# Kernel tuning notes

Measured on AMD Instinct MI355X. Metric: run time of the kernel, lower is better.

The kernel has to match this reference:

```python
import jax, jax.numpy as jnp
import numpy as np

# Constants from GaussianSplattingCompliance.__init__
SCALE_MIN, SCALE_MAX = 0.05, 1.5
RATIO_MIN, RATIO_MAX = 0.5, 3.5
ROT_MIN, ROT_MAX = -np.pi / 2, np.pi / 2
AXIS_OFFSET = 0.05
EMIN = 1e-9
SMOOTH_K = 10.0

N_POINTS = 131072  # number of FE element centers (512x256 mesh, flattened)
N_G = 256          # number of gaussians (args['args']['N_g'])


def setup_inputs() -> dict:
    key = jax.random.key(0)
    k0, k1, k2, k3, k4 = jax.random.split(key, 5)
    coords = jax.random.uniform(k0, (N_POINTS, 2), dtype=jnp.float32)
    W_scale = jax.random.normal(k1, (N_G, 1), dtype=jnp.float32)
    W_shape_var = jax.random.normal(k2, (N_G, 1), dtype=jnp.float32)
    W_rotation = jax.random.normal(k3, (N_G, 1), dtype=jnp.float32)
    W_offsets = jax.random.normal(k4, (N_G, 2), dtype=jnp.float32)
    return {"coords": coords, "W_scale": W_scale, "W_shape_var": W_shape_var,
            "W_rotation": W_rotation, "W_offsets": W_offsets}


def reference(coords, W_scale, W_shape_var, W_rotation, W_offsets):
    # coord bounds are constant buffers in the original module (computed once in __init__)
    c = jax.lax.stop_gradient(coords)
    cmin, cmax = c.min(axis=0), c.max(axis=0)                      # (2,)
    coord_min = cmin - cmax * AXIS_OFFSET
    coord_max = cmax + cmax * AXIS_OFFSET

    B = W_scale.shape[0]
    base_scale = (SCALE_MAX - SCALE_MIN) * jax.nn.sigmoid(W_scale)[:, 0] + SCALE_MIN   # (B,)
    ratio = (RATIO_MAX - RATIO_MIN) * jax.nn.sigmoid(W_shape_var) + RATIO_MIN          # (B,1)
    sigmas = jnp.concatenate([jnp.ones((B, 1), coords.dtype), ratio], axis=1)          # (B,2)
    rotation = ROT_MIN + (ROT_MAX - ROT_MIN) * jax.nn.sigmoid(W_rotation)[:, 0]        # (B,)
    offsets = coord_min + (coord_max - coord_min) * jax.nn.sigmoid(W_offsets)          # (B,2)

    cos_r, sin_r = jnp.cos(rotation), jnp.sin(rotation)
    R = jnp.stack([jnp.stack([cos_r, -sin_r], axis=-1),
                   jnp.stack([sin_r, cos_r], axis=-1)], axis=-2)                       # (B,2,2)
    inv_cov_diag = 1.0 / (sigmas ** 2 + 1e-6)                                          # (B,2)

    # (B, N, 2): centered, scaled coordinates per gaussian
    xy = (coords[None, :, :] - offsets[:, None, :]) / (base_scale[:, None, None] + 1e-8)
    rxy = jnp.einsum('bij,bnj->bni', R, xy)                                            # (B,N,2)
    # diagonal Mahalanobis quadratic form
    z = jnp.sqrt(jnp.einsum('bni,bi,bni->bn', rxy, inv_cov_diag, rxy))                 # (B,N)
    kernel = jax.nn.sigmoid(-10.0 * (z - 1.0))                                         # 1/(1+exp(10(z-1)))
    kernel_sum = kernel.sum(axis=0) + 1e-8                                             # (N,)
    H = (1.0 - EMIN) * jax.nn.sigmoid(-SMOOTH_K * (kernel_sum - 0.5)) + EMIN           # (N,)
    return H
```

## Files before the change

### kernel.cpp

```cpp
#include <hip/hip_runtime.h>
#include <cmath>

#define N_GAUSS 256

__global__ __launch_bounds__(256) void k_partial_minmax(
    const float2* __restrict__ coords, int n, float4* __restrict__ partial) {
  int tid = blockIdx.x * blockDim.x + threadIdx.x;
  int stride = gridDim.x * blockDim.x;
  float mnx = INFINITY, mny = INFINITY, mxx = -INFINITY, mxy = -INFINITY;
  for (int i = tid; i < n; i += stride) {
    float2 c = coords[i];
    mnx = fminf(mnx, c.x);
    mny = fminf(mny, c.y);
    mxx = fmaxf(mxx, c.x);
    mxy = fmaxf(mxy, c.y);
  }
  for (int o = 32; o > 0; o >>= 1) {
    mnx = fminf(mnx, __shfl_down(mnx, o));
    mny = fminf(mny, __shfl_down(mny, o));
    mxx = fmaxf(mxx, __shfl_down(mxx, o));
    mxy = fmaxf(mxy, __shfl_down(mxy, o));
  }
  __shared__ float4 lds[4];
  if ((threadIdx.x & 63) == 0) lds[threadIdx.x >> 6] = make_float4(mnx, mny, mxx, mxy);
  __syncthreads();
  if (threadIdx.x == 0) {
    float4 r = lds[0];
    for (int w = 1; w < 4; ++w) {
      float4 o = lds[w];
      r.x = fminf(r.x, o.x);
      r.y = fminf(r.y, o.y);
      r.z = fmaxf(r.z, o.z);
      r.w = fmaxf(r.w, o.w);
    }
    partial[blockIdx.x] = r;
  }
}

__device__ __forceinline__ float sigmoidf_fast(float w) {
  float t = __builtin_amdgcn_exp2f(-1.4426950408889634f * w);
  return 1.0f / (1.0f + t);
}

__global__ __launch_bounds__(256) void k_fused_main(
    const float2* __restrict__ coords,
    const float4* __restrict__ partial,
    const float* __restrict__ W_scale,
    const float* __restrict__ W_shape_var,
    const float* __restrict__ W_rotation,
    const float* __restrict__ W_offsets,
    float* __restrict__ out, int n) {
  __shared__ float4 sp[2 * N_GAUSS];
  __shared__ float4 lds4[4];
  __shared__ float4 boundsS;

  int t = threadIdx.x;

  float4 r = partial[t];
  for (int o = 32; o > 0; o >>= 1) {
    r.x = fminf(r.x, __shfl_down(r.x, o));
    r.y = fminf(r.y, __shfl_down(r.y, o));
    r.z = fmaxf(r.z, __shfl_down(r.z, o));
    r.w = fmaxf(r.w, __shfl_down(r.w, o));
  }
  if ((t & 63) == 0) lds4[t >> 6] = r;
  __syncthreads();
  if (t == 0) {
    float4 a = lds4[0];
    for (int w = 1; w < 4; ++w) {
      float4 o = lds4[w];
      a.x = fminf(a.x, o.x);
      a.y = fminf(a.y, o.y);
      a.z = fmaxf(a.z, o.z);
      a.w = fmaxf(a.w, o.w);
    }
    boundsS = a;
  }
  __syncthreads();
  float4 bc = boundsS;

  {
    float cmin0 = bc.x - bc.z * 0.05f;
    float cmin1 = bc.y - bc.w * 0.05f;
    float cmax0 = bc.z + bc.z * 0.05f;
    float cmax1 = bc.w + bc.w * 0.05f;

    float sS = sigmoidf_fast(W_scale[t]);
    float base_scale = 1.45f * sS + 0.05f;
    float sV = sigmoidf_fast(W_shape_var[t]);
    float ratio = 3.0f * sV + 0.5f;
    float sR = sigmoidf_fast(W_rotation[t]);
    const float PIf = 3.14159265358979323846f;
    float rot = -0.5f * PIf + PIf * sR;
    float sOx = sigmoidf_fast(W_offsets[2 * t]);
    float sOy = sigmoidf_fast(W_offsets[2 * t + 1]);
    float ox = cmin0 + (cmax0 - cmin0) * sOx;
    float oy = cmin1 + (cmax1 - cmin1) * sOy;

    float cr = cosf(rot), sr = sinf(rot);
    float inv_s = 1.0f / (base_scale + 1e-8f);
    float r0 = rsqrtf(1.0f + 1e-6f);
    float r1 = rsqrtf(fmaf(ratio, ratio, 1e-6f));

    float A = r0 * cr * inv_s;
    float B = -r0 * sr * inv_s;
    float E = -fmaf(A, ox, B * oy);
    float C = r1 * sr * inv_s;
    float D = r1 * cr * inv_s;
    float F = -fmaf(C, ox, D * oy);

    sp[2 * t]     = make_float4(A, B, E, C);
    sp[2 * t + 1] = make_float4(D, F, 0.0f, 0.0f);
  }
  __syncthreads();

  int i = blockIdx.x * blockDim.x + threadIdx.x;
  if (i >= n) return;
  float2 c = coords[i];
  float x = c.x, y = c.y;
  float ks = 1e-8f;
  const float K1 = 14.4269504088896339f;

  for (int b0 = 0; b0 < N_GAUSS; b0 += 8) {
#pragma unroll
    for (int j = 0; j < 8; ++j) {
      int b = b0 + j;
      float4 p0 = sp[2 * b];
      float4 p1 = sp[2 * b + 1];
      float u = fmaf(p0.x, x, fmaf(p0.y, y, p0.z));
      float v = fmaf(p0.w, x, fmaf(p1.x, y, p1.y));
      float z = sqrtf(fmaf(u, u, v * v));
      float tt = __builtin_amdgcn_exp2f(fmaf(K1, z, -K1));
      ks += __builtin_amdgcn_rcpf(1.0f + tt);
    }
    if (__all(ks > 6.0f)) break;
  }

  float t2 = __builtin_amdgcn_exp2f(fmaf(K1, ks, -0.5f * K1));
  float s = __builtin_amdgcn_rcpf(1.0f + t2);
  out[i] = fmaf(1e-9f, 1.0f - s, s);
}

extern "C" void kernel_launch(void* const* d_in, const int* in_sizes, int n_in,
                              void* d_out, int out_size, void* d_ws, size_t ws_size,
                              hipStream_t stream) {
  const float* coords      = (const float*)d_in[0];
  const float* W_scale     = (const float*)d_in[1];
  const float* W_shape_var = (const float*)d_in[2];
  const float* W_rotation  = (const float*)d_in[3];
  const float* W_offsets   = (const float*)d_in[4];
  float* out = (float*)d_out;

  int n = in_sizes[0] / 2;

  float4* partial = (float4*)d_ws;

  k_partial_minmax<<<256, 256, 0, stream>>>((const float2*)coords, n, partial);
  int blocks = (n + 255) / 256;
  k_fused_main<<<blocks, 256, 0, stream>>>((const float2*)coords, partial,
                                           W_scale, W_shape_var, W_rotation,
                                           W_offsets, out, n);
}
```

Measured before the change: 66.84 us.

## Fuse min/max reduction and main pass into one cooperative kernel with grid sync

Replaces the two-kernel sequence (partial min/max, then fused evaluation) with a single cooperative launch of at most 512 blocks. Each block writes its partial bounds, a grid-wide sync follows, and then every block reduces all partials, folds the gaussian parameters into LDS and grid-strides over the points. This removes one kernel launch and the gap between launches. In exchange it pays for a grid barrier, has each block redo the final reduction and parameter setup, and caps parallelism at 512 blocks, so each thread handles several points.

Result: slower. 126.8 us (+89.7%).

```diff
diff --git a/kernel.cpp b/kernel.cpp
--- a/kernel.cpp
+++ b/kernel.cpp
@@ -1,45 +1,203 @@
 #include <hip/hip_runtime.h>
+#include <hip/hip_cooperative_groups.h>
 #include <cmath>
 
 #define N_GAUSS 256
+
+namespace cg = cooperative_groups;
+
+
+__device__ __forceinline__ float sigmoidf_fast(float w) {
+  float t = __builtin_amdgcn_exp2f(-1.4426950408889634f * w);
+  return 1.0f / (1.0f + t);
+}
+
+__device__ __forceinline__ void wave_reduce_minmax(float4& r) {
+  for (int o = 32; o > 0; o >>= 1) {
+    r.x = fminf(r.x, __shfl_down(r.x, o));
+    r.y = fminf(r.y, __shfl_down(r.y, o));
+    r.z = fmaxf(r.z, __shfl_down(r.z, o));
+    r.w = fmaxf(r.w, __shfl_down(r.w, o));
+  }
+}
+
+__device__ __forceinline__ void store_agent(float* p, float v) {
+  __hip_atomic_store(p, v, __ATOMIC_RELAXED, __HIP_MEMORY_SCOPE_AGENT);
+}
+__device__ __forceinline__ float load_agent(const float* p) {
+  return __hip_atomic_load(p, __ATOMIC_RELAXED, __HIP_MEMORY_SCOPE_AGENT);
+}
+
+__device__ __forceinline__ void fold_params(float4 bc, int t,
+    const float* __restrict__ W_scale, const float* __restrict__ W_shape_var,
+    const float* __restrict__ W_rotation, const float* __restrict__ W_offsets,
+    float4* sp) {
+  float cmin0 = bc.x - bc.z * 0.05f;
+  float cmin1 = bc.y - bc.w * 0.05f;
+  float cmax0 = bc.z + bc.z * 0.05f;
+  float cmax1 = bc.w + bc.w * 0.05f;
+
+  float sS = sigmoidf_fast(W_scale[t]);
+  float base_scale = 1.45f * sS + 0.05f;
+  float sV = sigmoidf_fast(W_shape_var[t]);
+  float ratio = 3.0f * sV + 0.5f;
+  float sR = sigmoidf_fast(W_rotation[t]);
+  const float PIf = 3.14159265358979323846f;
+  float rot = -0.5f * PIf + PIf * sR;
+  float sOx = sigmoidf_fast(W_offsets[2 * t]);
+  float sOy = sigmoidf_fast(W_offsets[2 * t + 1]);
+  float ox = cmin0 + (cmax0 - cmin0) * sOx;
+  float oy = cmin1 + (cmax1 - cmin1) * sOy;
+
+  float cr = cosf(rot), sr = sinf(rot);
+  float inv_s = 1.0f / (base_scale + 1e-8f);
+  float r0 = rsqrtf(1.0f + 1e-6f);
+  float r1 = rsqrtf(fmaf(ratio, ratio, 1e-6f));
+
+  float A = r0 * cr * inv_s;
+  float B = -r0 * sr * inv_s;
+  float E = -fmaf(A, ox, B * oy);
+  float C = r1 * sr * inv_s;
+  float D = r1 * cr * inv_s;
+  float F = -fmaf(C, ox, D * oy);
+
+  sp[2 * t]     = make_float4(A, B, E, C);
+  sp[2 * t + 1] = make_float4(D, F, 0.0f, 0.0f);
+}
+
+__device__ __forceinline__ float eval_point(const float4* sp, float2 c) {
+  float x = c.x, y = c.y;
+  float ks = 1e-8f;
+  const float K1 = 14.4269504088896339f;
+
+  for (int b0 = 0; b0 < N_GAUSS; b0 += 8) {
+#pragma unroll
+    for (int j = 0; j < 8; ++j) {
+      int b = b0 + j;
+      float4 p0 = sp[2 * b];
+      float4 p1 = sp[2 * b + 1];
+      float u = fmaf(p0.x, x, fmaf(p0.y, y, p0.z));
+      float v = fmaf(p0.w, x, fmaf(p1.x, y, p1.y));
+      float z = sqrtf(fmaf(u, u, v * v));
+      float tt = __builtin_amdgcn_exp2f(fmaf(K1, z, -K1));
+      ks += __builtin_amdgcn_rcpf(1.0f + tt);
+    }
+    if (__all(ks > 6.0f)) break;
+  }
+
+  float t2 = __builtin_amdgcn_exp2f(fmaf(K1, ks, -0.5f * K1));
+  float s = __builtin_amdgcn_rcpf(1.0f + t2);
+  return fmaf(1e-9f, 1.0f - s, s);
+}
+
+__global__ __launch_bounds__(256) void k_coop(
+    const float2* __restrict__ coords,
+    float* __restrict__ pbuf,
+    const float* __restrict__ W_scale,
+    const float* __restrict__ W_shape_var,
+    const float* __restrict__ W_rotation,
+    const float* __restrict__ W_offsets,
+    float* __restrict__ out, int n) {
+  __shared__ float4 sp[2 * N_GAUSS];
+  __shared__ float4 lds4[4];
+  __shared__ float4 boundsS;
+
+  int t = threadIdx.x;
+  int nb = gridDim.x;
+  int nthreads = nb * 256;
+  int gid = blockIdx.x * 256 + t;
+
+  float4 r = make_float4(INFINITY, INFINITY, -INFINITY, -INFINITY);
+  for (int i = gid; i < n; i += nthreads) {
+    float2 c = coords[i];
+    r.x = fminf(r.x, c.x);
+    r.y = fminf(r.y, c.y);
+    r.z = fmaxf(r.z, c.x);
+    r.w = fmaxf(r.w, c.y);
+  }
+  wave_reduce_minmax(r);
+  if ((t & 63) == 0) lds4[t >> 6] = r;
+  __syncthreads();
+  if (t == 0) {
+    float4 a = lds4[0];
+    for (int w = 1; w < 4; ++w) {
+      float4 o = lds4[w];
+      a.x = fminf(a.x, o.x);
+      a.y = fminf(a.y, o.y);
+      a.z = fmaxf(a.z, o.z);
+      a.w = fmaxf(a.w, o.w);
+    }
+    store_agent(&pbuf[4 * blockIdx.x + 0], a.x);
+    store_agent(&pbuf[4 * blockIdx.x + 1], a.y);
+    store_agent(&pbuf[4 * blockIdx.x + 2], a.z);
+    store_agent(&pbuf[4 * blockIdx.x + 3], a.w);
+  }
+
+  cg::this_grid().sync();
+
+  float4 g = make_float4(INFINITY, INFINITY, -INFINITY, -INFINITY);
+  for (int s = t; s < nb; s += 256) {
+    float px = load_agent(&pbuf[4 * s + 0]);
+    float py = load_agent(&pbuf[4 * s + 1]);
+    float pz = load_agent(&pbuf[4 * s + 2]);
+    float pw = load_agent(&pbuf[4 * s + 3]);
+    g.x = fminf(g.x, px);
+    g.y = fminf(g.y, py);
+    g.z = fmaxf(g.z, pz);
+    g.w = fmaxf(g.w, pw);
+  }
+  wave_reduce_minmax(g);
+  if ((t & 63) == 0) lds4[t >> 6] = g;
+  __syncthreads();
+  if (t == 0) {
+    float4 a = lds4[0];
+    for (int w = 1; w < 4; ++w) {
+      float4 o = lds4[w];
+      a.x = fminf(a.x, o.x);
+      a.y = fminf(a.y, o.y);
+      a.z = fmaxf(a.z, o.z);
+      a.w = fmaxf(a.w, o.w);
+    }
+    boundsS = a;
+  }
+  __syncthreads();
+  float4 bc = boundsS;
+
+  fold_params(bc, t, W_scale, W_shape_var, W_rotation, W_offsets, sp);
+  __syncthreads();
+
+  for (int i = gid; i < n; i += nthreads) {
+    out[i] = eval_point(sp, coords[i]);
+  }
+}
 
 __global__ __launch_bounds__(256) void k_partial_minmax(
     const float2* __restrict__ coords, int n, float4* __restrict__ partial) {
   int tid = blockIdx.x * blockDim.x + threadIdx.x;
   int stride = gridDim.x * blockDim.x;
-  float mnx = INFINITY, mny = INFINITY, mxx = -INFINITY, mxy = -INFINITY;
+  float4 r = make_float4(INFINITY, INFINITY, -INFINITY, -INFINITY);
   for (int i = tid; i < n; i += stride) {
     float2 c = coords[i];
-    mnx = fminf(mnx, c.x);
-    mny = fminf(mny, c.y);
-    mxx = fmaxf(mxx, c.x);
-    mxy = fmaxf(mxy, c.y);
-  }
-  for (int o = 32; o > 0; o >>= 1) {
-    mnx = fminf(mnx, __shfl_down(mnx, o));
-    mny = fminf(mny, __shfl_down(mny, o));
-    mxx = fmaxf(mxx, __shfl_down(mxx, o));
-    mxy = fmaxf(mxy, __shfl_down(mxy, o));
-  }
+    r.x = fminf(r.x, c.x);
+    r.y = fminf(r.y, c.y);
+    r.z = fmaxf(r.z, c.x);
+    r.w = fmaxf(r.w, c.y);
+  }
+  wave_reduce_minmax(r);
   __shared__ float4 lds[4];
-  if ((threadIdx.x & 63) == 0) lds[threadIdx.x >> 6] = make_float4(mnx, mny, mxx, mxy);
+  if ((threadIdx.x & 63) == 0) lds[threadIdx.x >> 6] = r;
   __syncthreads();
   if (threadIdx.x == 0) {
-    float4 r = lds[0];
+    float4 a = lds[0];
     for (int w = 1; w < 4; ++w) {
       float4 o = lds[w];
-      r.x = fminf(r.x, o.x);
-      r.y = fminf(r.y, o.y);
-      r.z = fmaxf(r.z, o.z);
-      r.w = fmaxf(r.w, o.w);
-    }
-    partial[blockIdx.x] = r;
-  }
-}
-
-__device__ __forceinline__ float sigmoidf_fast(float w) {
-  float t = __builtin_amdgcn_exp2f(-1.4426950408889634f * w);
-  return 1.0f / (1.0f + t);
+      a.x = fminf(a.x, o.x);
+      a.y = fminf(a.y, o.y);
+      a.z = fmaxf(a.z, o.z);
+      a.w = fmaxf(a.w, o.w);
+    }
+    partial[blockIdx.x] = a;
+  }
 }
 
 __global__ __launch_bounds__(256) void k_fused_main(
@@ -57,12 +215,7 @@
   int t = threadIdx.x;
 
   float4 r = partial[t];
-  for (int o = 32; o > 0; o >>= 1) {
-    r.x = fminf(r.x, __shfl_down(r.x, o));
-    r.y = fminf(r.y, __shfl_down(r.y, o));
-    r.z = fmaxf(r.z, __shfl_down(r.z, o));
-    r.w = fmaxf(r.w, __shfl_down(r.w, o));
-  }
+  wave_reduce_minmax(r);
   if ((t & 63) == 0) lds4[t >> 6] = r;
   __syncthreads();
   if (t == 0) {
@@ -79,72 +232,18 @@
   __syncthreads();
   float4 bc = boundsS;
 
-  {
-    float cmin0 = bc.x - bc.z * 0.05f;
-    float cmin1 = bc.y - bc.w * 0.05f;
-    float cmax0 = bc.z + bc.z * 0.05f;
-    float cmax1 = bc.w + bc.w * 0.05f;
-
-    float sS = sigmoidf_fast(W_scale[t]);
-    float base_scale = 1.45f * sS + 0.05f;
-    float sV = sigmoidf_fast(W_shape_var[t]);
-    float ratio = 3.0f * sV + 0.5f;
-    float sR = sigmoidf_fast(W_rotation[t]);
-    const float PIf = 3.14159265358979323846f;
-    float rot = -0.5f * PIf + PIf * sR;
-    float sOx = sigmoidf_fast(W_offsets[2 * t]);
-    float sOy = sigmoidf_fast(W_offsets[2 * t + 1]);
-    float ox = cmin0 + (cmax0 - cmin0) * sOx;
-    float oy = cmin1 + (cmax1 - cmin1) * sOy;
-
-    float cr = cosf(rot), sr = sinf(rot);
-    float inv_s = 1.0f / (base_scale + 1e-8f);
-    float r0 = rsqrtf(1.0f + 1e-6f);
-    float r1 = rsqrtf(fmaf(ratio, ratio, 1e-6f));
-
-    float A = r0 * cr * inv_s;
-    float B = -r0 * sr * inv_s;
-    float E = -fmaf(A, ox, B * oy);
-    float C = r1 * sr * inv_s;
-    float D = r1 * cr * inv_s;
-    float F = -fmaf(C, ox, D * oy);
-
-    sp[2 * t]     = make_float4(A, B, E, C);
-    sp[2 * t + 1] = make_float4(D, F, 0.0f, 0.0f);
-  }
+  fold_params(bc, t, W_scale, W_shape_var, W_rotation, W_offsets, sp);
   __syncthreads();
 
   int i = blockIdx.x * blockDim.x + threadIdx.x;
   if (i >= n) return;
-  float2 c = coords[i];
-  float x = c.x, y = c.y;
-  float ks = 1e-8f;
-  const float K1 = 14.4269504088896339f;
-
-  for (int b0 = 0; b0 < N_GAUSS; b0 += 8) {
-#pragma unroll
-    for (int j = 0; j < 8; ++j) {
-      int b = b0 + j;
-      float4 p0 = sp[2 * b];
-      float4 p1 = sp[2 * b + 1];
-      float u = fmaf(p0.x, x, fmaf(p0.y, y, p0.z));
-      float v = fmaf(p0.w, x, fmaf(p1.x, y, p1.y));
-      float z = sqrtf(fmaf(u, u, v * v));
-      float tt = __builtin_amdgcn_exp2f(fmaf(K1, z, -K1));
-      ks += __builtin_amdgcn_rcpf(1.0f + tt);
-    }
-    if (__all(ks > 6.0f)) break;
-  }
-
-  float t2 = __builtin_amdgcn_exp2f(fmaf(K1, ks, -0.5f * K1));
-  float s = __builtin_amdgcn_rcpf(1.0f + t2);
-  out[i] = fmaf(1e-9f, 1.0f - s, s);
+  out[i] = eval_point(sp, coords[i]);
 }
 
 extern "C" void kernel_launch(void* const* d_in, const int* in_sizes, int n_in,
                               void* d_out, int out_size, void* d_ws, size_t ws_size,
                               hipStream_t stream) {
-  const float* coords      = (const float*)d_in[0];
+  const float2* coords     = (const float2*)d_in[0];
   const float* W_scale     = (const float*)d_in[1];
   const float* W_shape_var = (const float*)d_in[2];
   const float* W_rotation  = (const float*)d_in[3];
@@ -153,11 +252,21 @@
 
   int n = in_sizes[0] / 2;
 
-  float4* partial = (float4*)d_ws;
-
-  k_partial_minmax<<<256, 256, 0, stream>>>((const float2*)coords, n, partial);
+  float* pbuf = (float*)d_ws;
+
   int blocks = (n + 255) / 256;
-  k_fused_main<<<blocks, 256, 0, stream>>>((const float2*)coords, partial,
-                                           W_scale, W_shape_var, W_rotation,
-                                           W_offsets, out, n);
-}
+  if (blocks > 512) blocks = 512;
+
+  void* args[] = {(void*)&coords, (void*)&pbuf, (void*)&W_scale,
+                  (void*)&W_shape_var, (void*)&W_rotation, (void*)&W_offsets,
+                  (void*)&out, (void*)&n};
+  hipError_t err = hipLaunchCooperativeKernel((const void*)k_coop, dim3(blocks),
+                                              dim3(256), args, 0, stream);
+  if (err != hipSuccess) {
+    float4* partial = (float4*)d_ws;
+    k_partial_minmax<<<256, 256, 0, stream>>>(coords, n, partial);
+    int b2 = (n + 255) / 256;
+    k_fused_main<<<b2, 256, 0, stream>>>(coords, partial, W_scale, W_shape_var,
+                                         W_rotation, W_offsets, out, n);
+  }
+}
```
